# Kernel optimization log

Measured on AMD Instinct MI355X. Metric: run time of the kernel, lower is better.

Reference implementation:

```python
import math
import jax, jax.numpy as jnp
import numpy as np

B, N, DQ, DK, DV, H = 8, 1024, 256, 256, 256, 8
EPS_SM = 1e-15
EPS_LN = 1e-5


def _layer_norm(x, g, b):
    mu = jnp.mean(x, axis=-1, keepdims=True)
    var = jnp.mean((x - mu) ** 2, axis=-1, keepdims=True)
    return (x - mu) * jax.lax.rsqrt(var + EPS_LN) * g + b


def setup_inputs() -> dict:
    key = jax.random.key(0)
    ks = jax.random.split(key, 16)
    s = 0.05
    inp = {
        "Q": jax.random.normal(ks[0], (B, N, DQ), jnp.float32),
        "K": jax.random.normal(ks[1], (B, N, DK), jnp.float32),
        "lengths": jnp.clip(jax.random.randint(ks[2], (B,), 0, N), 1, N),
        "Wq": jax.random.normal(ks[3], (DQ, DV), jnp.float32) * s,
        "bq": jnp.zeros((DV,), jnp.float32),
        "Wk": jax.random.normal(ks[4], (DK, DV), jnp.float32) * s,
        "bk": jnp.zeros((DV,), jnp.float32),
        "Wv": jax.random.normal(ks[5], (DK, DV), jnp.float32) * s,
        "bv": jnp.zeros((DV,), jnp.float32),
        "Wo": jax.random.normal(ks[6], (DV, DV), jnp.float32) * s,
        "bo": jnp.zeros((DV,), jnp.float32),
        "g0": jnp.ones((DV,), jnp.float32),
        "b0": jnp.zeros((DV,), jnp.float32),
        "g1": jnp.ones((DV,), jnp.float32),
        "b1": jnp.zeros((DV,), jnp.float32),
    }
    return inp


def reference(Q, K, lengths, Wq, bq, Wk, bk, Wv, bv, Wo, bo, g0, b0, g1, b1):
    d = DV // H  # head dim
    mask = (jnp.arange(N) < lengths[:, None]).astype(Q.dtype)  # (B, N)
    q = (Q @ Wq + bq) * mask[..., None]  # (B, N, DV)
    k = (K @ Wk + bk) * mask[..., None]
    v = (K @ Wv + bv) * mask[..., None]
    qh = q.reshape(B, N, H, d)
    kh = k.reshape(B, N, H, d)
    vh = v.reshape(B, N, H, d)
    # NB: original scales by sqrt(dim_V), not sqrt(head_dim)
    scores = jnp.einsum("bnhd,bmhd->bhnm", qh, kh) / math.sqrt(DV)
    # set_softmax: raw exp, mask rows and cols by lengths, normalize over keys
    e = jnp.exp(scores) * mask[:, None, :, None] * mask[:, None, None, :]
    A = e / (jnp.sum(e, axis=-1, keepdims=True) + EPS_SM)  # (B, H, N, N)
    O = qh + jnp.einsum("bhnm,bmhd->bnhd", A, vh)  # residual per head
    O = O.reshape(B, N, DV)
    O = _layer_norm(O, g0, b0)
    O = O + jax.nn.relu(O @ Wo + bo)
    O = _layer_norm(O, g1, b1)
    return O
```

## Files before the change

### kernel.cpp

```cpp
#include <hip/hip_runtime.h>
#include <hip/hip_bf16.h>


typedef __attribute__((ext_vector_type(8))) short short8;
typedef __attribute__((ext_vector_type(4))) short short4v;
typedef __attribute__((ext_vector_type(4))) float f32x4;

__device__ __forceinline__ short f2bf(float f) {
    union { float f; unsigned u; } x; x.f = f;
    unsigned r = x.u + 0x7fffu + ((x.u >> 16) & 1u);
    return (short)(r >> 16);
}
__device__ __forceinline__ float bf2f(short s) {
    union { unsigned u; float f; } x; x.u = ((unsigned)(unsigned short)s) << 16;
    return x.f;
}

__global__ __launch_bounds__(256) void wtrans_kernel(
    const float* __restrict__ Wq, const float* __restrict__ Wk,
    const float* __restrict__ Wv, const float* __restrict__ Wo,
    short* __restrict__ WqT, short* __restrict__ WkT,
    short* __restrict__ WvT, short* __restrict__ WoT)
{
    __shared__ short tile[64][72];
    const float* W; short* T;
    switch (blockIdx.y) {
        case 0:  W = Wq; T = WqT; break;
        case 1:  W = Wk; T = WkT; break;
        case 2:  W = Wv; T = WvT; break;
        default: W = Wo; T = WoT; break;
    }
    const int k0 = (blockIdx.x >> 2) * 64;
    const int n0 = (blockIdx.x & 3) * 64;
    const int c  = threadIdx.x & 63;
    const int r4 = threadIdx.x >> 6;
    #pragma unroll
    for (int i = 0; i < 16; i++) {
        int k = r4 + i * 4;
        tile[k][c] = f2bf(W[(size_t)(k0 + k) * 256 + n0 + c]);
    }
    __syncthreads();
    #pragma unroll
    for (int i = 0; i < 16; i++) {
        int n = r4 + i * 4;
        T[(size_t)(n0 + n) * 256 + k0 + c] = tile[c][n];
    }
}

__global__ __launch_bounds__(256) void proj_kernel(
    const float* __restrict__ Q, const float* __restrict__ Kin,
    const short* __restrict__ WqT, const short* __restrict__ WkT, const short* __restrict__ WvT,
    const float* __restrict__ bq, const float* __restrict__ bk, const float* __restrict__ bv,
    const int* __restrict__ lengths,
    short* __restrict__ qb, short* __restrict__ kb, short* __restrict__ vT)
{
    const int which = blockIdx.y;
    const float* A    = (which == 0) ? Q   : Kin;
    const short* WT   = (which == 0) ? WqT : (which == 1) ? WkT : WvT;
    const float* bias = (which == 0) ? bq  : (which == 1) ? bk  : bv;

    const int tid = threadIdx.x;
    const int lane = tid & 63, wid = tid >> 6;
    const int m = lane & 15, quad = lane >> 4;
    const int rh = wid >> 1, ch = wid & 1;
    const int r0 = blockIdx.x * 32 + rh * 16;
    const int c0 = ch * 128;
    const int b = blockIdx.x >> 5;
    const int len = lengths[b];
    const int ntok0 = r0 & 1023;

    f32x4 acc[8];
    #pragma unroll
    for (int t = 0; t < 8; t++) acc[t] = (f32x4){0.f, 0.f, 0.f, 0.f};

    if (ntok0 < len) {
        const float* arow = A + (size_t)(r0 + m) * 256;
        for (int kk = 0; kk < 256; kk += 32) {
            const float* ap = arow + kk + quad * 8;
            float4 f0 = *(const float4*)(ap);
            float4 f1 = *(const float4*)(ap + 4);
            short8 af;
            af[0] = f2bf(f0.x); af[1] = f2bf(f0.y); af[2] = f2bf(f0.z); af[3] = f2bf(f0.w);
            af[4] = f2bf(f1.x); af[5] = f2bf(f1.y); af[6] = f2bf(f1.z); af[7] = f2bf(f1.w);
            #pragma unroll
            for (int t = 0; t < 8; t++) {
                short8 bf = *(const short8*)(WT + (c0 + t * 16 + m) * 256 + kk + quad * 8);
                acc[t] = __builtin_amdgcn_mfma_f32_16x16x32_bf16(af, bf, acc[t], 0, 0, 0);
            }
        }
    }

    #pragma unroll
    for (int t = 0; t < 8; t++) {
        int n = c0 + t * 16 + m;
        float bv_ = bias[n];
        int h = n >> 5, i = n & 31;
        int bh = b * 8 + h;
        #pragma unroll
        for (int reg = 0; reg < 4; reg++) {
            int ntok = ntok0 + quad * 4 + reg;
            float val = (ntok < len) ? (acc[t][reg] + bv_) : 0.f;
            short s = f2bf(val);
            if (which == 2) {
                vT[(size_t)(bh * 32 + i) * 1024 + ntok] = s;
            } else {
                short* dst = (which == 0) ? qb : kb;
                dst[((size_t)bh * 1024 + ntok) * 32 + i] = s;
            }
        }
    }
}

__global__ __launch_bounds__(256) void attn_kernel(
    const short* __restrict__ qb, const short* __restrict__ kb, const short* __restrict__ vT,
    const int* __restrict__ lengths, float* __restrict__ O1)
{
    __shared__ short P[4][16][72];
    __shared__ float cbO[2][16][33];
    __shared__ float cbL[2][16];
    const int tid = threadIdx.x;
    const int lane = tid & 63, wid = tid >> 6;
    const int m = lane & 15, quad = lane >> 4;
    const int ks = wid & 1, qh = wid >> 1;
    const int bh = blockIdx.y;
    const int b = bh >> 3, h = bh & 7;
    const int len = lengths[b];
    const int qr0 = blockIdx.x * 32 + qh * 16;

    const short* qbase = qb + (size_t)bh * 1024 * 32;
    const short* kbase = kb + (size_t)bh * 1024 * 32;
    const short* vbase = vT + (size_t)bh * 32 * 1024;

    const short8 qf = *(const short8*)(qbase + (qr0 + m) * 32 + quad * 8);

    f32x4 o0 = (f32x4){0.f, 0.f, 0.f, 0.f};
    f32x4 o1 = (f32x4){0.f, 0.f, 0.f, 0.f};
    float l[4] = {0.f, 0.f, 0.f, 0.f};

    const int kbeg = ks * 512;
    int kchunks = 0;
    if (qr0 < len && len > kbeg) {
        int rem = len - kbeg;
        kchunks = rem >= 512 ? 8 : ((rem + 63) >> 6);
    }

    for (int ci = 0; ci < kchunks; ci++) {
        int key0 = kbeg + ci * 64;
        short8 vf0a = *(const short8*)(vbase + (size_t)(m) * 1024      + key0 + quad * 8);
        short8 vf1a = *(const short8*)(vbase + (size_t)(16 + m) * 1024 + key0 + quad * 8);
        short8 vf0b = *(const short8*)(vbase + (size_t)(m) * 1024      + key0 + 32 + quad * 8);
        short8 vf1b = *(const short8*)(vbase + (size_t)(16 + m) * 1024 + key0 + 32 + quad * 8);
        #pragma unroll
        for (int t = 0; t < 4; t++) {
            short8 kf = *(const short8*)(kbase + (key0 + t * 16 + m) * 32 + quad * 8);
            f32x4 s = __builtin_amdgcn_mfma_f32_16x16x32_bf16(qf, kf,
                        (f32x4){0.f, 0.f, 0.f, 0.f}, 0, 0, 0);
            int col = key0 + t * 16 + m;
            bool cm = col < len;
            #pragma unroll
            for (int reg = 0; reg < 4; reg++) {
                float e = cm ? __expf(s[reg] * 0.0625f) : 0.f;
                l[reg] += e;
                P[wid][quad * 4 + reg][t * 16 + m] = f2bf(e);
            }
        }
        asm volatile("s_waitcnt lgkmcnt(0)" ::: "memory");
        short8 pf0 = *(const short8*)(&P[wid][m][quad * 8]);
        short8 pf1 = *(const short8*)(&P[wid][m][32 + quad * 8]);
        o0 = __builtin_amdgcn_mfma_f32_16x16x32_bf16(pf0, vf0a, o0, 0, 0, 0);
        o1 = __builtin_amdgcn_mfma_f32_16x16x32_bf16(pf0, vf1a, o1, 0, 0, 0);
        o0 = __builtin_amdgcn_mfma_f32_16x16x32_bf16(pf1, vf0b, o0, 0, 0, 0);
        o1 = __builtin_amdgcn_mfma_f32_16x16x32_bf16(pf1, vf1b, o1, 0, 0, 0);
    }

    #pragma unroll
    for (int reg = 0; reg < 4; reg++) {
        float s = l[reg];
        s += __shfl_xor(s, 1); s += __shfl_xor(s, 2);
        s += __shfl_xor(s, 4); s += __shfl_xor(s, 8);
        l[reg] = s;
    }

    if (ks == 1) {
        #pragma unroll
        for (int reg = 0; reg < 4; reg++) {
            cbO[qh][quad * 4 + reg][m]      = o0[reg];
            cbO[qh][quad * 4 + reg][16 + m] = o1[reg];
        }
        if (m == 0) {
            #pragma unroll
            for (int reg = 0; reg < 4; reg++) cbL[qh][quad * 4 + reg] = l[reg];
        }
    }
    __syncthreads();
    if (ks == 0) {
        const int hbase = h * 32;
        #pragma unroll
        for (int reg = 0; reg < 4; reg++) {
            int r = quad * 4 + reg;
            o0[reg] += cbO[qh][r][m];
            o1[reg] += cbO[qh][r][16 + m];
            float lt = l[reg] + cbL[qh][r];
            int qrow = qr0 + r;
            float f = (qrow < len) ? 1.f / (lt + 1e-15f) : 0.f;
            size_t obase = ((size_t)(b * 1024 + qrow)) * 256 + hbase;
            float q0 = bf2f(qbase[qrow * 32 + m]);
            float q1 = bf2f(qbase[qrow * 32 + 16 + m]);
            O1[obase + m]      = q0 + o0[reg] * f;
            O1[obase + 16 + m] = q1 + o1[reg] * f;
        }
    }
}

__global__ __launch_bounds__(256) void out_kernel(
    const float* __restrict__ O1, const short* __restrict__ WoT,
    const float* __restrict__ g0, const float* __restrict__ b0,
    const float* __restrict__ bo, const float* __restrict__ g1, const float* __restrict__ b1,
    float* __restrict__ out)
{
    __shared__ short Xs[16][264];
    __shared__ float st[4][2][16];
    const int tid = threadIdx.x;
    const int r0 = blockIdx.x * 16;

    {
        const int lrow  = tid >> 4;
        const int cbase = (tid & 15) * 16;
        const float* rowp = O1 + (size_t)(r0 + lrow) * 256 + cbase;
        float4 a0 = ((const float4*)rowp)[0];
        float4 a1 = ((const float4*)rowp)[1];
        float4 a2 = ((const float4*)rowp)[2];
        float4 a3 = ((const float4*)rowp)[3];
        float s  = a0.x + a0.y + a0.z + a0.w + a1.x + a1.y + a1.z + a1.w
                 + a2.x + a2.y + a2.z + a2.w + a3.x + a3.y + a3.z + a3.w;
        float s2 = a0.x*a0.x + a0.y*a0.y + a0.z*a0.z + a0.w*a0.w
                 + a1.x*a1.x + a1.y*a1.y + a1.z*a1.z + a1.w*a1.w
                 + a2.x*a2.x + a2.y*a2.y + a2.z*a2.z + a2.w*a2.w
                 + a3.x*a3.x + a3.y*a3.y + a3.z*a3.z + a3.w*a3.w;
        s  += __shfl_xor(s, 1);  s  += __shfl_xor(s, 2);
        s  += __shfl_xor(s, 4);  s  += __shfl_xor(s, 8);
        s2 += __shfl_xor(s2, 1); s2 += __shfl_xor(s2, 2);
        s2 += __shfl_xor(s2, 4); s2 += __shfl_xor(s2, 8);
        float mean = s * (1.f / 256.f);
        float var  = s2 * (1.f / 256.f) - mean * mean;
        float rs = rsqrtf(var + 1e-5f);
        float4 g0a = ((const float4*)(g0 + cbase))[0];
        float4 g0b = ((const float4*)(g0 + cbase))[1];
        float4 g0c = ((const float4*)(g0 + cbase))[2];
        float4 g0d = ((const float4*)(g0 + cbase))[3];
        float4 b0a = ((const float4*)(b0 + cbase))[0];
        float4 b0b = ((const float4*)(b0 + cbase))[1];
        float4 b0c = ((const float4*)(b0 + cbase))[2];
        float4 b0d = ((const float4*)(b0 + cbase))[3];
        short8 y0, y1;
        y0[0] = f2bf((a0.x - mean) * rs * g0a.x + b0a.x);
        y0[1] = f2bf((a0.y - mean) * rs * g0a.y + b0a.y);
        y0[2] = f2bf((a0.z - mean) * rs * g0a.z + b0a.z);
        y0[3] = f2bf((a0.w - mean) * rs * g0a.w + b0a.w);
        y0[4] = f2bf((a1.x - mean) * rs * g0b.x + b0b.x);
        y0[5] = f2bf((a1.y - mean) * rs * g0b.y + b0b.y);
        y0[6] = f2bf((a1.z - mean) * rs * g0b.z + b0b.z);
        y0[7] = f2bf((a1.w - mean) * rs * g0b.w + b0b.w);
        y1[0] = f2bf((a2.x - mean) * rs * g0c.x + b0c.x);
        y1[1] = f2bf((a2.y - mean) * rs * g0c.y + b0c.y);
        y1[2] = f2bf((a2.z - mean) * rs * g0c.z + b0c.z);
        y1[3] = f2bf((a2.w - mean) * rs * g0c.w + b0c.w);
        y1[4] = f2bf((a3.x - mean) * rs * g0d.x + b0d.x);
        y1[5] = f2bf((a3.y - mean) * rs * g0d.y + b0d.y);
        y1[6] = f2bf((a3.z - mean) * rs * g0d.z + b0d.z);
        y1[7] = f2bf((a3.w - mean) * rs * g0d.w + b0d.w);
        *(short8*)(&Xs[lrow][cbase])     = y0;
        *(short8*)(&Xs[lrow][cbase + 8]) = y1;
    }
    __syncthreads();

    const int lane = tid & 63, wid = tid >> 6;
    const int m = lane & 15, quad = lane >> 4;
    const int c0 = wid * 64;

    f32x4 acc[4];
    #pragma unroll
    for (int t = 0; t < 4; t++) acc[t] = (f32x4){0.f, 0.f, 0.f, 0.f};

    for (int kk = 0; kk < 256; kk += 32) {
        short8 af = *(const short8*)(&Xs[m][kk + quad * 8]);
        #pragma unroll
        for (int t = 0; t < 4; t++) {
            short8 bf = *(const short8*)(WoT + (c0 + t * 16 + m) * 256 + kk + quad * 8);
            acc[t] = __builtin_amdgcn_mfma_f32_16x16x32_bf16(af, bf, acc[t], 0, 0, 0);
        }
    }

    float s1[4] = {0.f, 0.f, 0.f, 0.f};
    float s2v[4] = {0.f, 0.f, 0.f, 0.f};
    #pragma unroll
    for (int t = 0; t < 4; t++) {
        int n = c0 + t * 16 + m;
        float bon = bo[n];
        #pragma unroll
        for (int reg = 0; reg < 4; reg++) {
            int r = quad * 4 + reg;
            float xv = bf2f(Xs[r][n]);
            float c = acc[t][reg] + bon;
            float yv = xv + (c > 0.f ? c : 0.f);
            acc[t][reg] = yv;
            s1[reg] += yv;
            s2v[reg] += yv * yv;
        }
    }
    #pragma unroll
    for (int reg = 0; reg < 4; reg++) {
        float a = s1[reg], bsum = s2v[reg];
        a += __shfl_xor(a, 1); a += __shfl_xor(a, 2); a += __shfl_xor(a, 4); a += __shfl_xor(a, 8);
        bsum += __shfl_xor(bsum, 1); bsum += __shfl_xor(bsum, 2); bsum += __shfl_xor(bsum, 4); bsum += __shfl_xor(bsum, 8);
        s1[reg] = a; s2v[reg] = bsum;
    }
    if (m == 0) {
        #pragma unroll
        for (int reg = 0; reg < 4; reg++) {
            st[wid][0][quad * 4 + reg] = s1[reg];
            st[wid][1][quad * 4 + reg] = s2v[reg];
        }
    }
    __syncthreads();
    #pragma unroll
    for (int reg = 0; reg < 4; reg++) {
        int r = quad * 4 + reg;
        float t1 = st[0][0][r] + st[1][0][r] + st[2][0][r] + st[3][0][r];
        float t2 = st[0][1][r] + st[1][1][r] + st[2][1][r] + st[3][1][r];
        float mean = t1 * (1.f / 256.f);
        float var  = t2 * (1.f / 256.f) - mean * mean;
        float rs = rsqrtf(var + 1e-5f);
        int token = r0 + r;
        #pragma unroll
        for (int t = 0; t < 4; t++) {
            int n = c0 + t * 16 + m;
            out[(size_t)token * 256 + n] = (acc[t][reg] - mean) * rs * g1[n] + b1[n];
        }
    }
}

extern "C" void kernel_launch(void* const* d_in, const int* in_sizes, int n_in,
                              void* d_out, int out_size, void* d_ws, size_t ws_size,
                              hipStream_t stream) {
    const float* Q   = (const float*)d_in[0];
    const float* K   = (const float*)d_in[1];
    const int* lengths = (const int*)d_in[2];
    const float* Wq  = (const float*)d_in[3];
    const float* bq  = (const float*)d_in[4];
    const float* Wk  = (const float*)d_in[5];
    const float* bk  = (const float*)d_in[6];
    const float* Wv  = (const float*)d_in[7];
    const float* bv  = (const float*)d_in[8];
    const float* Wo  = (const float*)d_in[9];
    const float* bo  = (const float*)d_in[10];
    const float* g0  = (const float*)d_in[11];
    const float* b0  = (const float*)d_in[12];
    const float* g1  = (const float*)d_in[13];
    const float* b1  = (const float*)d_in[14];
    float* out = (float*)d_out;

    char* ws = (char*)d_ws;
    short* qb  = (short*)(ws);
    short* kb  = (short*)(ws + (4u << 20));
    short* vT  = (short*)(ws + (8u << 20));
    float* O1  = (float*)(ws + (12u << 20));
    short* WqT = (short*)(ws + (20u << 20));
    short* WkT = (short*)(ws + (20u << 20) + (128u << 10));
    short* WvT = (short*)(ws + (20u << 20) + (256u << 10));
    short* WoT = (short*)(ws + (20u << 20) + (384u << 10));

    wtrans_kernel<<<dim3(16, 4), 256, 0, stream>>>(Wq, Wk, Wv, Wo, WqT, WkT, WvT, WoT);
    proj_kernel<<<dim3(256, 3), 256, 0, stream>>>(Q, K, WqT, WkT, WvT, bq, bk, bv,
                                                  lengths, qb, kb, vT);
    attn_kernel<<<dim3(32, 64), 256, 0, stream>>>(qb, kb, vT, lengths, O1);
    out_kernel<<<dim3(512), 256, 0, stream>>>(O1, WoT, g0, b0, bo, g1, b1, out);
}
```

Before: 164.0 us.

## Fuse K and V projections and interleave attention key chunks across splits

The projection kernel now computes K and V together in one block, so K input rows are loaded and converted to bf16 once instead of twice, and the grid shrinks from three slices to two. This doubles accumulator registers for the K/V blocks, which may lower occupancy and leaves the Q and K/V blocks with unequal work. The attention kernel now hands alternating 64-key chunks to its two key-split waves instead of contiguous halves, which balances work when the valid length is below 512 and no longer idles one split.

Result: faster. 159.7 us (-2.6%).

```diff
diff --git a/kernel.cpp b/kernel.cpp
--- a/kernel.cpp
+++ b/kernel.cpp
@@ -55,9 +55,8 @@
     short* __restrict__ qb, short* __restrict__ kb, short* __restrict__ vT)
 {
     const int which = blockIdx.y;
-    const float* A    = (which == 0) ? Q   : Kin;
-    const short* WT   = (which == 0) ? WqT : (which == 1) ? WkT : WvT;
-    const float* bias = (which == 0) ? bq  : (which == 1) ? bk  : bv;
+    const float* A   = (which == 0) ? Q   : Kin;
+    const short* WTa = (which == 0) ? WqT : WkT;
 
     const int tid = threadIdx.x;
     const int lane = tid & 63, wid = tid >> 6;
@@ -69,9 +68,12 @@
     const int len = lengths[b];
     const int ntok0 = r0 & 1023;
 
-    f32x4 acc[8];
-    #pragma unroll
-    for (int t = 0; t < 8; t++) acc[t] = (f32x4){0.f, 0.f, 0.f, 0.f};
+    f32x4 accA[8], accB[8];
+    #pragma unroll
+    for (int t = 0; t < 8; t++) {
+        accA[t] = (f32x4){0.f, 0.f, 0.f, 0.f};
+        accB[t] = (f32x4){0.f, 0.f, 0.f, 0.f};
+    }
 
     if (ntok0 < len) {
         const float* arow = A + (size_t)(r0 + m) * 256;
@@ -84,8 +86,15 @@
             af[4] = f2bf(f1.x); af[5] = f2bf(f1.y); af[6] = f2bf(f1.z); af[7] = f2bf(f1.w);
             #pragma unroll
             for (int t = 0; t < 8; t++) {
-                short8 bf = *(const short8*)(WT + (c0 + t * 16 + m) * 256 + kk + quad * 8);
-                acc[t] = __builtin_amdgcn_mfma_f32_16x16x32_bf16(af, bf, acc[t], 0, 0, 0);
+                short8 bfa = *(const short8*)(WTa + (c0 + t * 16 + m) * 256 + kk + quad * 8);
+                accA[t] = __builtin_amdgcn_mfma_f32_16x16x32_bf16(af, bfa, accA[t], 0, 0, 0);
+            }
+            if (which == 1) {
+                #pragma unroll
+                for (int t = 0; t < 8; t++) {
+                    short8 bfb = *(const short8*)(WvT + (c0 + t * 16 + m) * 256 + kk + quad * 8);
+                    accB[t] = __builtin_amdgcn_mfma_f32_16x16x32_bf16(af, bfb, accB[t], 0, 0, 0);
+                }
             }
         }
     }
@@ -93,19 +102,27 @@
     #pragma unroll
     for (int t = 0; t < 8; t++) {
         int n = c0 + t * 16 + m;
-        float bv_ = bias[n];
         int h = n >> 5, i = n & 31;
         int bh = b * 8 + h;
-        #pragma unroll
-        for (int reg = 0; reg < 4; reg++) {
-            int ntok = ntok0 + quad * 4 + reg;
-            float val = (ntok < len) ? (acc[t][reg] + bv_) : 0.f;
-            short s = f2bf(val);
-            if (which == 2) {
-                vT[(size_t)(bh * 32 + i) * 1024 + ntok] = s;
-            } else {
-                short* dst = (which == 0) ? qb : kb;
-                dst[((size_t)bh * 1024 + ntok) * 32 + i] = s;
+        if (which == 0) {
+            float bias = bq[n];
+            #pragma unroll
+            for (int reg = 0; reg < 4; reg++) {
+                int ntok = ntok0 + quad * 4 + reg;
+                float val = (ntok < len) ? (accA[t][reg] + bias) : 0.f;
+                qb[((size_t)bh * 1024 + ntok) * 32 + i] = f2bf(val);
+            }
+        } else {
+            float bk_ = bk[n];
+            float bv_ = bv[n];
+            #pragma unroll
+            for (int reg = 0; reg < 4; reg++) {
+                int ntok = ntok0 + quad * 4 + reg;
+                bool ok = ntok < len;
+                float vk = ok ? (accA[t][reg] + bk_) : 0.f;
+                float vv = ok ? (accB[t][reg] + bv_) : 0.f;
+                kb[((size_t)bh * 1024 + ntok) * 32 + i] = f2bf(vk);
+                vT[(size_t)(bh * 32 + i) * 1024 + ntok] = f2bf(vv);
             }
         }
     }
@@ -137,15 +154,12 @@
     f32x4 o1 = (f32x4){0.f, 0.f, 0.f, 0.f};
     float l[4] = {0.f, 0.f, 0.f, 0.f};
 
-    const int kbeg = ks * 512;
-    int kchunks = 0;
-    if (qr0 < len && len > kbeg) {
-        int rem = len - kbeg;
-        kchunks = rem >= 512 ? 8 : ((rem + 63) >> 6);
-    }
+    int nch = 0;
+    if (qr0 < len) nch = (len + 63) >> 6;
+    const int kchunks = (nch + 1 - ks) >> 1;
 
     for (int ci = 0; ci < kchunks; ci++) {
-        int key0 = kbeg + ci * 64;
+        int key0 = (ci * 2 + ks) * 64;
         short8 vf0a = *(const short8*)(vbase + (size_t)(m) * 1024      + key0 + quad * 8);
         short8 vf1a = *(const short8*)(vbase + (size_t)(16 + m) * 1024 + key0 + quad * 8);
         short8 vf0b = *(const short8*)(vbase + (size_t)(m) * 1024      + key0 + 32 + quad * 8);
@@ -371,7 +385,7 @@
     short* WoT = (short*)(ws + (20u << 20) + (384u << 10));
 
     wtrans_kernel<<<dim3(16, 4), 256, 0, stream>>>(Wq, Wk, Wv, Wo, WqT, WkT, WvT, WoT);
-    proj_kernel<<<dim3(256, 3), 256, 0, stream>>>(Q, K, WqT, WkT, WvT, bq, bk, bv,
+    proj_kernel<<<dim3(256, 2), 256, 0, stream>>>(Q, K, WqT, WkT, WvT, bq, bk, bv,
                                                   lengths, qb, kb, vT);
     attn_kernel<<<dim3(32, 64), 256, 0, stream>>>(qb, kb, vT, lengths, O1);
     out_kernel<<<dim3(512), 256, 0, stream>>>(O1, WoT, g0, b0, bo, g1, b1, out);
```
